# Optimization experiments

Hardware: AMD Instinct MI355X
Metric: run time of the kernel (lower is better)

Reference implementation:

```python
import jax, jax.numpy as jnp
import numpy as np

RELU_NEG_SLOPE = 0.2

def _gat_layer(x, W, a, src, dst, num_nodes, concat):
    # x: [N, Din]; W: [H, Din, F]; a: [H, 2F]; src/dst: [E]
    H, _, F = W.shape
    proj = jnp.einsum('nd,hdf->nhf', x, W)              # [N, H, F]
    a_self, a_nb = a[:, :F], a[:, F:]                   # [H, F] each
    alpha_self = jnp.einsum('nhf,hf->nh', proj, a_self) # [N, H]
    alpha_nb = jnp.einsum('nhf,hf->nh', proj, a_nb)     # [N, H]
    # edge score: a . [proj_dst || proj_src], dst = center node i, src = neighbor j
    e = jax.nn.leaky_relu(alpha_self[dst] + alpha_nb[src], RELU_NEG_SLOPE)  # [E, H]
    e_max = jax.ops.segment_max(e, dst, num_segments=num_nodes)
    e_exp = jnp.exp(e - e_max[dst])
    denom = jax.ops.segment_sum(e_exp, dst, num_segments=num_nodes)
    w = e_exp / denom[dst]                              # [E, H] softmax per dst node
    msg = proj[src] * w[:, :, None]                     # [E, H, F]
    out = jax.ops.segment_sum(msg, dst, num_segments=num_nodes)  # [N, H, F]
    if concat:
        return out.reshape(num_nodes, H * F)
    return out.mean(axis=1)


def setup_inputs() -> dict:
    key = jax.random.key(0)
    k1, k2, k3, k4, k5, k6 = jax.random.split(key, 6)
    N, Din, F1, H1 = 10000, 128, 64, 8
    Dmid = H1 * F1  # 512
    F2, H2 = 64, 1
    x = jax.random.normal(k1, (N, Din), dtype=jnp.float32)
    edges = jax.random.randint(k2, (2, 80000), 0, N, dtype=jnp.int64)
    W1 = jax.random.normal(k3, (H1, Din, F1), dtype=jnp.float32) / np.sqrt(Din)
    a1 = jax.random.normal(k4, (H1, 2 * F1), dtype=jnp.float32) / np.sqrt(2 * F1)
    W2 = jax.random.normal(k5, (H2, Dmid, F2), dtype=jnp.float32) / np.sqrt(Dmid)
    a2 = jax.random.normal(k6, (H2, 2 * F2), dtype=jnp.float32) / np.sqrt(2 * F2)
    return {"x": x, "edges": edges, "W1": W1, "a1": a1, "W2": W2, "a2": a2}


def reference(x, edges, W1, a1, W2, a2):
    N = x.shape[0]
    loops = jnp.arange(N, dtype=edges.dtype)
    # undirected graph + self loops (Graph.neighborhood adds both directions and self)
    src = jnp.concatenate([edges[0], edges[1], loops])
    dst = jnp.concatenate([edges[1], edges[0], loops])
    h = _gat_layer(x, W1, a1, src, dst, N, concat=True)   # [N, 512]
    h = jax.nn.elu(h)
    out = _gat_layer(h, W2, a2, src, dst, N, concat=False)  # [N, 64]
    return out
```

## Files before the change

kernel.cpp:

```cpp
#include <hip/hip_runtime.h>
#include <hip/hip_bf16.h>
#include <hip/hip_fp16.h>

#define RELU_NEG_SLOPE 0.2f

typedef _Float16 half8 __attribute__((ext_vector_type(8)));
typedef float f32x4 __attribute__((ext_vector_type(4)));

__device__ __forceinline__ float leaky(float e) {
    return (e > 0.f) ? e : RELU_NEG_SLOPE * e;
}

__device__ __forceinline__ float elu1(float x) {
    return (x > 0.f) ? x : (__expf(x) - 1.f);
}

__global__ __launch_bounds__(256) void stage_kernel(
    const float4* __restrict__ x4, const float* __restrict__ W1,
    const float* __restrict__ W2, float2* __restrict__ xh,
    __half* __restrict__ Bt1, __half* __restrict__ W2t,
    int* __restrict__ cnt, int n4, int t1, int t2, int N) {
    int i = blockIdx.x * 256 + threadIdx.x;
    if (i < n4) {
        float4 v = x4[i];
        float2 p;
        ((__half2*)&p)[0] = __floats2half2_rn(v.x, v.y);
        ((__half2*)&p)[1] = __floats2half2_rn(v.z, v.w);
        xh[i] = p;
    } else if (i < n4 + t1) {
        int j = i - n4;
        int f = j & 63;
        int d = (j >> 6) & 127;
        int h = j >> 13;
        Bt1[((h * 64 + f) << 7) + d] = __float2half(W1[j]);
    } else if (i < n4 + t1 + t2) {
        int j = i - n4 - t1;
        int f = j & 63;
        int d = j >> 6;
        W2t[f * 512 + d] = __float2half(W2[j]);
    } else if (i < n4 + t1 + t2 + N) {
        cnt[i - n4 - t1 - t2] = 0;
    }
}

__global__ __launch_bounds__(256) void scatter_gemm1(
    const int* __restrict__ edges, int E0, int* __restrict__ cnt,
    int* __restrict__ ell, int nscat,
    const __half* __restrict__ Ah, const __half* __restrict__ Bt,
    const float* __restrict__ a1, __half* __restrict__ Cp,
    float* __restrict__ as_, float* __restrict__ an_, int M, int slabN) {
    if (blockIdx.x < nscat) {
        int i = blockIdx.x * 256 + threadIdx.x;
        if (i >= 2 * E0) return;
        int s = edges[i];
        int d = (i < E0) ? edges[E0 + i] : edges[i - E0];
        int pos = atomicAdd(&cnt[d], 1);
        ell[(d << 6) + pos] = s;
        return;
    }
    int bid2 = blockIdx.x - nscat;
    const int h = bid2 & 7;
    const int by = bid2 >> 3;
    const int lane = threadIdx.x & 63;
    const int wave = threadIdx.x >> 6;
    const int q = lane >> 4;
    const int l15 = lane & 15;
    const int mrow = by * 64 + wave * 16;

    f32x4 acc[4] = {{0.f, 0.f, 0.f, 0.f}, {0.f, 0.f, 0.f, 0.f},
                    {0.f, 0.f, 0.f, 0.f}, {0.f, 0.f, 0.f, 0.f}};
    const __half* Ap = Ah + (size_t)(mrow + l15) * 128 + q * 8;
    const __half* Bp = Bt + (size_t)(h * 64 + l15) * 128 + q * 8;
#pragma unroll
    for (int ks = 0; ks < 4; ks++) {
        half8 av = *(const half8*)(Ap + ks * 32);
#pragma unroll
        for (int t = 0; t < 4; t++) {
            half8 bv = *(const half8*)(Bp + (size_t)t * 16 * 128 + ks * 32);
            acc[t] = __builtin_amdgcn_mfma_f32_16x16x32_f16(av, bv, acc[t], 0, 0, 0);
        }
    }

    __half* Cs = Cp + (size_t)(h >> 1) * slabN + (h & 1) * 64;
    float asc[4], anc[4];
#pragma unroll
    for (int t = 0; t < 4; t++) {
        asc[t] = a1[h * 128 + t * 16 + l15];
        anc[t] = a1[h * 128 + 64 + t * 16 + l15];
    }
#pragma unroll
    for (int r = 0; r < 4; r++) {
        int mg = mrow + q * 4 + r;
        float ps = 0.f, pn = 0.f;
#pragma unroll
        for (int t = 0; t < 4; t++) {
            float v = acc[t][r];
            ps += v * asc[t];
            pn += v * anc[t];
            if (mg < M)
                Cs[(size_t)mg * 128 + t * 16 + l15] = __float2half(v);
        }
#pragma unroll
        for (int m = 8; m >= 1; m >>= 1) {
            ps += __shfl_xor(ps, m, 64);
            pn += __shfl_xor(pn, m, 64);
        }
        if (l15 == 0 && mg < M) {
            as_[mg * 8 + h] = ps;
            an_[mg * 8 + h] = pn;
        }
    }
}

__global__ __launch_bounds__(256) void agg_h8_sliced(
    const int* __restrict__ cnt, const int* __restrict__ ell,
    const __half* __restrict__ projp, const float* __restrict__ as_,
    const float* __restrict__ an_, __half* __restrict__ outh,
    int N, int slabN) {
    int bid = blockIdx.x;
    int hp = bid & 3;
    int rem = bid >> 2;
    int d = rem * 4 + (threadIdx.x >> 6);
    int lane = threadIdx.x & 63;
    if (d >= N) return;
    const int sub = lane >> 3;
    const int inner = lane & 7;
    const int hh = inner >> 2;
    const int h = hp * 2 + hh;
    const int c16 = (inner & 3) * 16;

    int deg = cnt[d];
    const int* row = ell + (d << 6);
    float asd = as_[d * 8 + h];
    const __half* slab = projp + (size_t)hp * slabN;

    float acc[16];
#pragma unroll
    for (int i = 0; i < 16; i++) acc[i] = 0.f;
    float den = 0.f;
    if (sub == 0) {
        float e = __expf(leaky(asd + an_[d * 8 + h]));
        const __half* p = slab + (size_t)d * 128 + hh * 64 + c16;
        half8 v0 = *(const half8*)p;
        half8 v1 = *(const half8*)(p + 8);
        den = e;
#pragma unroll
        for (int i = 0; i < 8; i++) {
            acc[i] = e * (float)v0[i];
            acc[8 + i] = e * (float)v1[i];
        }
    }
    for (int j0 = 0; j0 < deg; j0 += 8) {
        int j = j0 + sub;
        int jc = (j < deg) ? j : (deg - 1);
        int s = row[jc];
        float e = __expf(leaky(asd + an_[s * 8 + h]));
        if (j >= deg) e = 0.f;
        const __half* p = slab + (size_t)s * 128 + hh * 64 + c16;
        half8 v0 = *(const half8*)p;
        half8 v1 = *(const half8*)(p + 8);
        den += e;
#pragma unroll
        for (int i = 0; i < 8; i++) {
            acc[i] += e * (float)v0[i];
            acc[8 + i] += e * (float)v1[i];
        }
    }

#pragma unroll
    for (int off = 32; off >= 8; off >>= 1) {
#pragma unroll
        for (int i = 0; i < 16; i++) acc[i] += __shfl_down(acc[i], off, 64);
        den += __shfl_down(den, off, 64);
    }

    if (sub == 0) {
        float r = 1.f / den;
        half8 o0, o1;
#pragma unroll
        for (int i = 0; i < 8; i++) {
            o0[i] = (_Float16)elu1(acc[i] * r);
            o1[i] = (_Float16)elu1(acc[8 + i] * r);
        }
        __half* op = outh + (size_t)d * 512 + h * 64 + c16;
        *(half8*)op = o0;
        *(half8*)(op + 8) = o1;
    }
}

__global__ __launch_bounds__(256) void mfma_gemm2(
    const __half* __restrict__ Ah, const __half* __restrict__ Bt,
    const float* __restrict__ a2, __half* __restrict__ Ch,
    float* __restrict__ as_, float* __restrict__ an_, int M) {
    const int lane = threadIdx.x & 63;
    const int wave = threadIdx.x >> 6;
    const int q = lane >> 4;
    const int l15 = lane & 15;
    const int mrow = blockIdx.x * 64 + wave * 16;

    f32x4 acc[4] = {{0.f, 0.f, 0.f, 0.f}, {0.f, 0.f, 0.f, 0.f},
                    {0.f, 0.f, 0.f, 0.f}, {0.f, 0.f, 0.f, 0.f}};
    const __half* Ap = Ah + (size_t)(mrow + l15) * 512 + q * 8;
    const __half* Bp = Bt + (size_t)l15 * 512 + q * 8;
#pragma unroll
    for (int ks = 0; ks < 16; ks++) {
        half8 av = *(const half8*)(Ap + ks * 32);
#pragma unroll
        for (int t = 0; t < 4; t++) {
            half8 bv = *(const half8*)(Bp + (size_t)t * 16 * 512 + ks * 32);
            acc[t] = __builtin_amdgcn_mfma_f32_16x16x32_f16(av, bv, acc[t], 0, 0, 0);
        }
    }

    float asc[4], anc[4];
#pragma unroll
    for (int t = 0; t < 4; t++) {
        asc[t] = a2[t * 16 + l15];
        anc[t] = a2[64 + t * 16 + l15];
    }
#pragma unroll
    for (int r = 0; r < 4; r++) {
        int mg = mrow + q * 4 + r;
        float ps = 0.f, pn = 0.f;
#pragma unroll
        for (int t = 0; t < 4; t++) {
            float v = acc[t][r];
            ps += v * asc[t];
            pn += v * anc[t];
            if (mg < M)
                Ch[(size_t)mg * 64 + t * 16 + l15] = __float2half(v);
        }
#pragma unroll
        for (int m = 8; m >= 1; m >>= 1) {
            ps += __shfl_xor(ps, m, 64);
            pn += __shfl_xor(pn, m, 64);
        }
        if (l15 == 0 && mg < M) {
            as_[mg] = ps;
            an_[mg] = pn;
        }
    }
}

__global__ __launch_bounds__(256) void agg_node_h1(
    const int* __restrict__ cnt, const int* __restrict__ ell,
    const __half* __restrict__ projh, const float* __restrict__ as_,
    const float* __restrict__ an_, float* __restrict__ out, int N) {
    int d = blockIdx.x * 4 + (threadIdx.x >> 6);
    int lane = threadIdx.x & 63;
    if (d >= N) return;
    int sub = lane >> 4;
    int fl = lane & 15;
    int deg = cnt[d];
    const int* row = ell + (d << 6);
    float asd = as_[d];

    float4 acc = make_float4(0.f, 0.f, 0.f, 0.f);
    float den = 0.f;
    for (int j0 = 0; j0 < deg; j0 += 4) {
        int j = j0 + sub;
        int jc = (j < deg) ? j : (deg - 1);
        int s = row[jc];
        float e = __expf(leaky(asd + an_[s]));
        if (j >= deg) e = 0.f;
        float2 raw = *(const float2*)(projh + (size_t)s * 64 + fl * 4);
        float2 p01 = __half22float2(*(__half2*)&raw.x);
        float2 p23 = __half22float2(*(__half2*)&raw.y);
        den += e;
        acc.x += e * p01.x;
        acc.y += e * p01.y;
        acc.z += e * p23.x;
        acc.w += e * p23.y;
    }

#pragma unroll
    for (int off = 32; off >= 16; off >>= 1) {
        acc.x += __shfl_down(acc.x, off, 64);
        acc.y += __shfl_down(acc.y, off, 64);
        acc.z += __shfl_down(acc.z, off, 64);
        acc.w += __shfl_down(acc.w, off, 64);
        den += __shfl_down(den, off, 64);
    }

    if (sub == 0) {
        float e = __expf(leaky(asd + an_[d]));
        float2 raw = *(const float2*)(projh + (size_t)d * 64 + fl * 4);
        float2 p01 = __half22float2(*(__half2*)&raw.x);
        float2 p23 = __half22float2(*(__half2*)&raw.y);
        den += e;
        acc.x += e * p01.x;
        acc.y += e * p01.y;
        acc.z += e * p23.x;
        acc.w += e * p23.y;
        float rden = 1.f / den;
        float4 r;
        r.x = acc.x * rden;
        r.y = acc.y * rden;
        r.z = acc.z * rden;
        r.w = acc.w * rden;
        *(float4*)(out + (size_t)d * 64 + fl * 4) = r;
    }
}

extern "C" void kernel_launch(void* const* d_in, const int* in_sizes, int n_in,
                              void* d_out, int out_size, void* d_ws, size_t ws_size,
                              hipStream_t stream) {
    const float* x  = (const float*)d_in[0];
    const int* edges = (const int*)d_in[1];
    const float* W1 = (const float*)d_in[2];
    const float* a1 = (const float*)d_in[3];
    const float* W2 = (const float*)d_in[4];
    const float* a2 = (const float*)d_in[5];

    const int Din = 128, H1 = 8, F = 64, Dmid = 512;
    const int N = in_sizes[0] / Din;
    const int E0 = in_sizes[1] / 2;
    const int Mpad = (N + 63) & ~63;
    const int slabN = Mpad * 128;

    char* base = (char*)d_ws;
    size_t off = 0;
    auto take = [&](size_t bytes) {
        void* p = base + off;
        off = (off + bytes + 255) & ~(size_t)255;
        return p;
    };
    __half* x_h    = (__half*)take((size_t)Mpad * Din * 2);
    __half* proj1p = (__half*)take((size_t)4 * slabN * 2);
    __half* hbufh  = (__half*)take((size_t)Mpad * Dmid * 2);
    __half* proj2h = (__half*)take((size_t)N * F * 2);
    __half* Bt1    = (__half*)take((size_t)Dmid * Din * 2);
    __half* W2t    = (__half*)take((size_t)F * Dmid * 2);
    float* as1 = (float*)take((size_t)N * H1 * 4);
    float* an1 = (float*)take((size_t)N * H1 * 4);
    float* as2 = (float*)take((size_t)N * 4);
    float* an2 = (float*)take((size_t)N * 4);
    int* cnt = (int*)take((size_t)N * 4);
    int* ell = (int*)take((size_t)N * 64 * 4);

    int n4 = N * Din / 4;
    int t1 = H1 * Din * F, t2 = Dmid * F;
    int total = n4 + t1 + t2 + N;
    stage_kernel<<<(total + 255) / 256, 256, 0, stream>>>(
        (const float4*)x, W1, W2, (float2*)x_h, Bt1, W2t, cnt, n4, t1, t2, N);

    int nscat = (2 * E0 + 255) / 256;
    int ngemm = H1 * ((N + 63) / 64);
    scatter_gemm1<<<nscat + ngemm, 256, 0, stream>>>(
        edges, E0, cnt, ell, nscat,
        x_h, Bt1, a1, proj1p, as1, an1, N, slabN);

    int nbp = (N + 3) / 4;
    agg_h8_sliced<<<4 * nbp, 256, 0, stream>>>(cnt, ell, proj1p, as1, an1,
                                               hbufh, N, slabN);

    mfma_gemm2<<<(N + 63) / 64, 256, 0, stream>>>(hbufh, W2t, a2, proj2h,
                                                  as2, an2, N);

    agg_node_h1<<<(N + 3) / 4, 256, 0, stream>>>(cnt, ell, proj2h,
                                                 as2, an2, (float*)d_out, N);
}
```

Before: 143.7 us.

## Shrink ELL indices to 16-bit, use single-wave GEMM2 blocks, widen layer-2 gather

The ELL neighbor list now stores 16-bit source indices instead of 32-bit, halving the index traffic in both aggregation kernels. The second GEMM launches one 64-thread wave per block over 16 rows, giving more, smaller blocks. The layer-2 aggregation processes 8 neighbors per iteration with 16-byte half8 loads per lane. The 16-bit indices only hold for node counts up to 65535, so this depends on the input size.

```diff
diff --git a/kernel.cpp b/kernel.cpp
--- a/kernel.cpp
+++ b/kernel.cpp
@@ -45,7 +45,7 @@
 
 __global__ __launch_bounds__(256) void scatter_gemm1(
     const int* __restrict__ edges, int E0, int* __restrict__ cnt,
-    int* __restrict__ ell, int nscat,
+    unsigned short* __restrict__ ell, int nscat,
     const __half* __restrict__ Ah, const __half* __restrict__ Bt,
     const float* __restrict__ a1, __half* __restrict__ Cp,
     float* __restrict__ as_, float* __restrict__ an_, int M, int slabN) {
@@ -55,7 +55,7 @@
         int s = edges[i];
         int d = (i < E0) ? edges[E0 + i] : edges[i - E0];
         int pos = atomicAdd(&cnt[d], 1);
-        ell[(d << 6) + pos] = s;
+        ell[(d << 6) + pos] = (unsigned short)s;
         return;
     }
     int bid2 = blockIdx.x - nscat;
@@ -113,7 +113,7 @@
 }
 
 __global__ __launch_bounds__(256) void agg_h8_sliced(
-    const int* __restrict__ cnt, const int* __restrict__ ell,
+    const int* __restrict__ cnt, const unsigned short* __restrict__ ell,
     const __half* __restrict__ projp, const float* __restrict__ as_,
     const float* __restrict__ an_, __half* __restrict__ outh,
     int N, int slabN) {
@@ -130,7 +130,7 @@
     const int c16 = (inner & 3) * 16;
 
     int deg = cnt[d];
-    const int* row = ell + (d << 6);
+    const unsigned short* row = ell + (d << 6);
     float asd = as_[d * 8 + h];
     const __half* slab = projp + (size_t)hp * slabN;
 
@@ -188,15 +188,14 @@
     }
 }
 
-__global__ __launch_bounds__(256) void mfma_gemm2(
+__global__ __launch_bounds__(64) void mfma_gemm2(
     const __half* __restrict__ Ah, const __half* __restrict__ Bt,
     const float* __restrict__ a2, __half* __restrict__ Ch,
     float* __restrict__ as_, float* __restrict__ an_, int M) {
     const int lane = threadIdx.x & 63;
-    const int wave = threadIdx.x >> 6;
     const int q = lane >> 4;
     const int l15 = lane & 15;
-    const int mrow = blockIdx.x * 64 + wave * 16;
+    const int mrow = blockIdx.x * 16;
 
     f32x4 acc[4] = {{0.f, 0.f, 0.f, 0.f}, {0.f, 0.f, 0.f, 0.f},
                     {0.f, 0.f, 0.f, 0.f}, {0.f, 0.f, 0.f, 0.f}};
@@ -243,62 +242,56 @@
 }
 
 __global__ __launch_bounds__(256) void agg_node_h1(
-    const int* __restrict__ cnt, const int* __restrict__ ell,
+    const int* __restrict__ cnt, const unsigned short* __restrict__ ell,
     const __half* __restrict__ projh, const float* __restrict__ as_,
     const float* __restrict__ an_, float* __restrict__ out, int N) {
     int d = blockIdx.x * 4 + (threadIdx.x >> 6);
     int lane = threadIdx.x & 63;
     if (d >= N) return;
-    int sub = lane >> 4;
-    int fl = lane & 15;
+    int sub = lane >> 3;
+    int inner = lane & 7;
     int deg = cnt[d];
-    const int* row = ell + (d << 6);
+    const unsigned short* row = ell + (d << 6);
     float asd = as_[d];
 
-    float4 acc = make_float4(0.f, 0.f, 0.f, 0.f);
+    float acc[8];
+#pragma unroll
+    for (int i = 0; i < 8; i++) acc[i] = 0.f;
     float den = 0.f;
-    for (int j0 = 0; j0 < deg; j0 += 4) {
+    for (int j0 = 0; j0 < deg; j0 += 8) {
         int j = j0 + sub;
         int jc = (j < deg) ? j : (deg - 1);
         int s = row[jc];
         float e = __expf(leaky(asd + an_[s]));
         if (j >= deg) e = 0.f;
-        float2 raw = *(const float2*)(projh + (size_t)s * 64 + fl * 4);
-        float2 p01 = __half22float2(*(__half2*)&raw.x);
-        float2 p23 = __half22float2(*(__half2*)&raw.y);
+        half8 v = *(const half8*)(projh + (size_t)s * 64 + inner * 8);
         den += e;
-        acc.x += e * p01.x;
-        acc.y += e * p01.y;
-        acc.z += e * p23.x;
-        acc.w += e * p23.y;
-    }
-
-#pragma unroll
-    for (int off = 32; off >= 16; off >>= 1) {
-        acc.x += __shfl_down(acc.x, off, 64);
-        acc.y += __shfl_down(acc.y, off, 64);
-        acc.z += __shfl_down(acc.z, off, 64);
-        acc.w += __shfl_down(acc.w, off, 64);
+#pragma unroll
+        for (int i = 0; i < 8; i++) acc[i] += e * (float)v[i];
+    }
+
+#pragma unroll
+    for (int off = 32; off >= 8; off >>= 1) {
+#pragma unroll
+        for (int i = 0; i < 8; i++) acc[i] += __shfl_down(acc[i], off, 64);
         den += __shfl_down(den, off, 64);
     }
 
     if (sub == 0) {
         float e = __expf(leaky(asd + an_[d]));
-        float2 raw = *(const float2*)(projh + (size_t)d * 64 + fl * 4);
-        float2 p01 = __half22float2(*(__half2*)&raw.x);
-        float2 p23 = __half22float2(*(__half2*)&raw.y);
+        half8 v = *(const half8*)(projh + (size_t)d * 64 + inner * 8);
         den += e;
-        acc.x += e * p01.x;
-        acc.y += e * p01.y;
-        acc.z += e * p23.x;
-        acc.w += e * p23.y;
+#pragma unroll
+        for (int i = 0; i < 8; i++) acc[i] += e * (float)v[i];
         float rden = 1.f / den;
-        float4 r;
-        r.x = acc.x * rden;
-        r.y = acc.y * rden;
-        r.z = acc.z * rden;
-        r.w = acc.w * rden;
-        *(float4*)(out + (size_t)d * 64 + fl * 4) = r;
+        float4 r0, r1;
+        r0.x = acc[0] * rden; r0.y = acc[1] * rden;
+        r0.z = acc[2] * rden; r0.w = acc[3] * rden;
+        r1.x = acc[4] * rden; r1.y = acc[5] * rden;
+        r1.z = acc[6] * rden; r1.w = acc[7] * rden;
+        float* op = out + (size_t)d * 64 + inner * 8;
+        *(float4*)op = r0;
+        *(float4*)(op + 4) = r1;
     }
 }
 
@@ -336,7 +329,7 @@
     float* as2 = (float*)take((size_t)N * 4);
     float* an2 = (float*)take((size_t)N * 4);
     int* cnt = (int*)take((size_t)N * 4);
-    int* ell = (int*)take((size_t)N * 64 * 4);
+    unsigned short* ell = (unsigned short*)take((size_t)N * 64 * 2);
 
     int n4 = N * Din / 4;
     int t1 = H1 * Din * F, t2 = Dmid * F;
@@ -354,8 +347,8 @@
     agg_h8_sliced<<<4 * nbp, 256, 0, stream>>>(cnt, ell, proj1p, as1, an1,
                                                hbufh, N, slabN);
 
-    mfma_gemm2<<<(N + 63) / 64, 256, 0, stream>>>(hbufh, W2t, a2, proj2h,
-                                                  as2, an2, N);
+    mfma_gemm2<<<(N + 15) / 16, 64, 0, stream>>>(hbufh, W2t, a2, proj2h,
+                                                 as2, an2, N);
 
     agg_node_h1<<<(N + 3) / 4, 256, 0, stream>>>(cnt, ell, proj2h,
                                                  as2, an2, (float*)d_out, N);
```

Measured after the change: 140.0 us. -2.6%, faster.
